# Kernel optimization log

Measured on AMD Instinct MI355X. Metric: run time of the kernel, lower is better.

Reference implementation:

```python
import jax, jax.numpy as jnp
import numpy as np

B, V, P, A, NF = 32, 2048, 64, 8, 128
F = P + A          # concat of transformed features and aggregator weights
DIN = P + 2 * A * F + A  # final cat: orig + expanded_collapsed + agg


def setup_inputs() -> dict:
    key = jax.random.key(0)
    ks = jax.random.split(key, 7)
    s = lambda fan: 1.0 / np.sqrt(fan)
    return {
        "vertices_in": jax.random.normal(ks[0], (B, V, P), dtype=jnp.float32),
        "W1": jax.random.normal(ks[1], (P, P), dtype=jnp.float32) * s(P),
        "b1": jax.random.normal(ks[2], (P,), dtype=jnp.float32) * s(P),
        "W2": jax.random.normal(ks[3], (P, A), dtype=jnp.float32) * s(P),
        "b2": jax.random.normal(ks[4], (A,), dtype=jnp.float32) * s(P),
        "Wout": jax.random.normal(ks[5], (DIN, NF), dtype=jnp.float32) * s(DIN),
        "bout": jax.random.normal(ks[6], (NF,), dtype=jnp.float32) * s(DIN),
    }


def reference(vertices_in, W1, b1, W2, b2, Wout, bout):
    # vertices_in: [B,V,P]
    vi = vertices_in @ W1 + b1                              # [B,V,P]
    agg = jnp.exp(-jnp.abs(vertices_in @ W2 + b2))          # [B,V,A] gauss_of_lin
    feats = jnp.concatenate([vi, agg], axis=-1)             # [B,V,F]
    # edge weights e[b,a,v] = agg[b,v,a]; broadcast multiply then max/mean over V
    prod = jnp.transpose(agg, (0, 2, 1))[:, :, :, None] * feats[:, None, :, :]  # [B,A,V,F]
    mx = jnp.max(prod, axis=2)                              # [B,A,F]
    mn = jnp.mean(prod, axis=2)                             # [B,A,F]
    collapsed = jnp.concatenate([mx, mn], axis=-1)          # [B,A,2F]
    # expand back to vertices: e[b,v,a] * collapsed[b,a,g]
    expanded = agg[:, :, :, None] * collapsed[:, None, :, :]  # [B,V,A,2F]
    expanded = expanded.reshape(B, V, A * 2 * F)
    x = jnp.concatenate([vertices_in, expanded, agg], axis=-1)  # [B,V,DIN]
    return jnp.tanh(x @ Wout + bout)                        # [B,V,NF]
```

## Files before the change

kernel.cpp:

```cpp
#include <hip/hip_runtime.h>
#include <math.h>

#define BB 32
#define VV 2048
#define PP 64
#define AA 8
#define NFF 128
#define FF 72
#define TWOF 144

__global__ __launch_bounds__(256) void k1_feats(
        const float* __restrict__ x,
        const float* __restrict__ W1, const float* __restrict__ b1,
        const float* __restrict__ W2, const float* __restrict__ b2,
        float* __restrict__ featsT, float* __restrict__ agg) {
    const int b    = blockIdx.y;
    const int t    = threadIdx.x;
    const int w    = __builtin_amdgcn_readfirstlane(t >> 6);
    const int lane = t & 63;
    const int v    = blockIdx.x * 64 + lane;

    float xs[64];
    const float4* xp = reinterpret_cast<const float4*>(x + ((size_t)b * VV + v) * PP);
    #pragma unroll
    for (int i = 0; i < 16; ++i) {
        float4 t4 = xp[i];
        xs[4 * i + 0] = t4.x; xs[4 * i + 1] = t4.y; xs[4 * i + 2] = t4.z; xs[4 * i + 3] = t4.w;
    }

    #pragma unroll 1
    for (int k = 0; k < 5; ++k) {
        const int c = w + 4 * k;
        if (c >= 18) break;
        const int f0 = 4 * c;
        float4 acc;
        if (c < 16) {
            acc = make_float4(b1[f0 + 0], b1[f0 + 1], b1[f0 + 2], b1[f0 + 3]);
            #pragma unroll
            for (int p = 0; p < 64; ++p) {
                const float4 wt = *reinterpret_cast<const float4*>(&W1[p * 64 + f0]);
                const float xv = xs[p];
                acc.x += xv * wt.x; acc.y += xv * wt.y; acc.z += xv * wt.z; acc.w += xv * wt.w;
            }
        } else {
            const int a0 = f0 - 64;
            acc = make_float4(b2[a0 + 0], b2[a0 + 1], b2[a0 + 2], b2[a0 + 3]);
            #pragma unroll
            for (int p = 0; p < 64; ++p) {
                const float4 wt = *reinterpret_cast<const float4*>(&W2[p * 8 + a0]);
                const float xv = xs[p];
                acc.x += xv * wt.x; acc.y += xv * wt.y; acc.z += xv * wt.z; acc.w += xv * wt.w;
            }
            acc.x = __expf(-fabsf(acc.x));
            acc.y = __expf(-fabsf(acc.y));
            acc.z = __expf(-fabsf(acc.z));
            acc.w = __expf(-fabsf(acc.w));
            float4* ap = reinterpret_cast<float4*>(agg + ((size_t)b * VV + v) * AA);
            ap[c - 16] = acc;
        }
        float* fr = featsT + ((size_t)b * FF + f0) * VV + v;
        fr[0 * VV] = acc.x; fr[1 * VV] = acc.y; fr[2 * VV] = acc.z; fr[3 * VV] = acc.w;
    }
}

__global__ __launch_bounds__(256) void k2_reduce(
        const float* __restrict__ featsT, const float* __restrict__ agg,
        float* __restrict__ collapsed) {
    const int fg = blockIdx.x;
    const int b  = blockIdx.y;
    const int f0 = fg * 4;
    const int t  = threadIdx.x;
    const int wave = t >> 6, lane = t & 63;

    __shared__ float redm[4][32];
    __shared__ float reds[4][32];

    float pmax[4][8], psum[4][8];
    #pragma unroll
    for (int j = 0; j < 4; ++j)
        #pragma unroll
        for (int a = 0; a < 8; ++a) { pmax[j][a] = -INFINITY; psum[j][a] = 0.0f; }

    for (int i = 0; i < 8; ++i) {
        const int v = i * 256 + t;
        const float4* ep = reinterpret_cast<const float4*>(agg + ((size_t)b * VV + v) * AA);
        const float4 e0 = ep[0], e1 = ep[1];
        float e[8];
        e[0] = e0.x; e[1] = e0.y; e[2] = e0.z; e[3] = e0.w;
        e[4] = e1.x; e[5] = e1.y; e[6] = e1.z; e[7] = e1.w;
        #pragma unroll
        for (int j = 0; j < 4; ++j) {
            const float fv = featsT[((size_t)b * FF + f0 + j) * VV + v];
            #pragma unroll
            for (int a = 0; a < 8; ++a) {
                const float pr = e[a] * fv;
                pmax[j][a] = fmaxf(pmax[j][a], pr);
                psum[j][a] += pr;
            }
        }
    }

    #pragma unroll
    for (int j = 0; j < 4; ++j) {
        #pragma unroll
        for (int a = 0; a < 8; ++a) {
            float m = pmax[j][a];
            float s = psum[j][a];
            #pragma unroll
            for (int d = 1; d < 64; d <<= 1) {
                m = fmaxf(m, __shfl_xor(m, d));
                s += __shfl_xor(s, d);
            }
            if (lane == 0) { redm[wave][j * 8 + a] = m; reds[wave][j * 8 + a] = s; }
        }
    }
    __syncthreads();

    if (t < 32) {
        const int j = t >> 3, a = t & 7;
        float m = redm[0][t], s = reds[0][t];
        #pragma unroll
        for (int w = 1; w < 4; ++w) { m = fmaxf(m, redm[w][t]); s += reds[w][t]; }
        float* cr = collapsed + ((size_t)b * AA + a) * TWOF;
        cr[f0 + j]      = m;
        cr[FF + f0 + j] = s * (1.0f / (float)VV);
    }
}

__global__ __launch_bounds__(256) void k2b_mprime(
        const float* __restrict__ collapsed, const float* __restrict__ Wout,
        float* __restrict__ Mp) {
    const int a = blockIdx.x, b = blockIdx.y;
    const int t = threadIdx.x;
    const int nf = t & 127, gh = t >> 7;
    __shared__ float part[2][128];

    const float* col  = collapsed + ((size_t)b * AA + a) * TWOF;
    const float* Wexp = Wout + (size_t)(64 + a * TWOF) * NFF;

    float acc = 0.0f;
    const int g0 = gh * 72;
    #pragma unroll 8
    for (int g = g0; g < g0 + 72; ++g)
        acc += col[g] * Wexp[(size_t)g * NFF + nf];
    part[gh][nf] = acc;
    __syncthreads();

    if (t < 128) {
        float r = part[0][t] + part[1][t] + Wout[(size_t)(1216 + a) * NFF + t];
        Mp[((size_t)b * AA + a) * NFF + t] = r;
    }
}

__device__ __forceinline__ float fast_tanh(float z) {
    const float e = __expf(2.0f * z);
    return 1.0f - 2.0f / (e + 1.0f);
}

__global__ __launch_bounds__(256) void k3_out(
        const float* __restrict__ x, const float* __restrict__ agg,
        const float* __restrict__ Mp, const float* __restrict__ Wout,
        const float* __restrict__ bout, float* __restrict__ out) {
    const int b    = blockIdx.y;
    const int t    = threadIdx.x;
    const int q    = __builtin_amdgcn_readfirstlane(t >> 6);
    const int lane = t & 63;
    const int v    = blockIdx.x * 64 + lane;
    const int n0   = q * 32;

    float xs[64];
    const float4* xp = reinterpret_cast<const float4*>(x + ((size_t)b * VV + v) * PP);
    #pragma unroll
    for (int i = 0; i < 16; ++i) {
        float4 t4 = xp[i];
        xs[4 * i + 0] = t4.x; xs[4 * i + 1] = t4.y; xs[4 * i + 2] = t4.z; xs[4 * i + 3] = t4.w;
    }
    float e[8];
    const float4* ep = reinterpret_cast<const float4*>(agg + ((size_t)b * VV + v) * AA);
    {
        const float4 e0 = ep[0], e1 = ep[1];
        e[0] = e0.x; e[1] = e0.y; e[2] = e0.z; e[3] = e0.w;
        e[4] = e1.x; e[5] = e1.y; e[6] = e1.z; e[7] = e1.w;
    }

    const float* Wq  = Wout + n0;
    const float* Mpq = Mp + (size_t)b * AA * NFF + n0;
    const float* bq  = bout + n0;
    float* op = out + ((size_t)b * VV + v) * NFF + n0;

    #pragma unroll 1
    for (int cc = 0; cc < 8; ++cc) {
        float4 acc = make_float4(bq[4 * cc + 0], bq[4 * cc + 1],
                                 bq[4 * cc + 2], bq[4 * cc + 3]);
        #pragma unroll
        for (int p = 0; p < 64; ++p) {
            const float4 wt = *reinterpret_cast<const float4*>(&Wq[(size_t)p * NFF + 4 * cc]);
            const float xv = xs[p];
            acc.x += xv * wt.x; acc.y += xv * wt.y; acc.z += xv * wt.z; acc.w += xv * wt.w;
        }
        #pragma unroll
        for (int a = 0; a < 8; ++a) {
            const float4 wt = *reinterpret_cast<const float4*>(&Mpq[(size_t)a * NFF + 4 * cc]);
            const float ea = e[a];
            acc.x += ea * wt.x; acc.y += ea * wt.y; acc.z += ea * wt.z; acc.w += ea * wt.w;
        }
        acc.x = fast_tanh(acc.x); acc.y = fast_tanh(acc.y);
        acc.z = fast_tanh(acc.z); acc.w = fast_tanh(acc.w);
        *reinterpret_cast<float4*>(&op[4 * cc]) = acc;
    }
}

extern "C" void kernel_launch(void* const* d_in, const int* in_sizes, int n_in,
                              void* d_out, int out_size, void* d_ws, size_t ws_size,
                              hipStream_t stream) {
    const float* x    = (const float*)d_in[0];
    const float* W1   = (const float*)d_in[1];
    const float* b1   = (const float*)d_in[2];
    const float* W2   = (const float*)d_in[3];
    const float* b2   = (const float*)d_in[4];
    const float* Wout = (const float*)d_in[5];
    const float* bout = (const float*)d_in[6];
    float* out = (float*)d_out;

    float* ws     = (float*)d_ws;
    float* featsT = ws;
    float* agg    = featsT + (size_t)BB * FF * VV;
    float* coll   = agg + (size_t)BB * VV * AA;
    float* Mp     = coll + (size_t)BB * AA * TWOF;

    k1_feats<<<dim3(32, 32), dim3(256), 0, stream>>>(x, W1, b1, W2, b2, featsT, agg);
    k2_reduce<<<dim3(18, 32), dim3(256), 0, stream>>>(featsT, agg, coll);
    k2b_mprime<<<dim3(8, 32), dim3(256), 0, stream>>>(coll, Wout, Mp);
    k3_out<<<dim3(32, 32), dim3(256), 0, stream>>>(x, agg, Mp, Wout, bout, out);
}
```

Before: 169.9 us.

## Split V-reduction across two blocks and restructure output GEMM loop order

```diff
diff --git a/kernel.cpp b/kernel.cpp
--- a/kernel.cpp
+++ b/kernel.cpp
@@ -65,8 +65,10 @@
 
 __global__ __launch_bounds__(256) void k2_reduce(
         const float* __restrict__ featsT, const float* __restrict__ agg,
-        float* __restrict__ collapsed) {
-    const int fg = blockIdx.x;
+        float* __restrict__ part) {
+    const int bx = blockIdx.x;
+    const int fg = bx >> 1;
+    const int vh = bx & 1;
     const int b  = blockIdx.y;
     const int f0 = fg * 4;
     const int t  = threadIdx.x;
@@ -81,8 +83,8 @@
         #pragma unroll
         for (int a = 0; a < 8; ++a) { pmax[j][a] = -INFINITY; psum[j][a] = 0.0f; }
 
-    for (int i = 0; i < 8; ++i) {
-        const int v = i * 256 + t;
+    for (int i = 0; i < 4; ++i) {
+        const int v = vh * 1024 + i * 256 + t;
         const float4* ep = reinterpret_cast<const float4*>(agg + ((size_t)b * VV + v) * AA);
         const float4 e0 = ep[0], e1 = ep[1];
         float e[8];
@@ -121,33 +123,45 @@
         float m = redm[0][t], s = reds[0][t];
         #pragma unroll
         for (int w = 1; w < 4; ++w) { m = fmaxf(m, redm[w][t]); s += reds[w][t]; }
-        float* cr = collapsed + ((size_t)b * AA + a) * TWOF;
-        cr[f0 + j]      = m;
-        cr[FF + f0 + j] = s * (1.0f / (float)VV);
+        float* pr = part + (((size_t)vh * BB + b) * AA + a) * TWOF;
+        pr[f0 + j]      = m;
+        pr[FF + f0 + j] = s;
     }
 }
 
 __global__ __launch_bounds__(256) void k2b_mprime(
-        const float* __restrict__ collapsed, const float* __restrict__ Wout,
+        const float* __restrict__ part, const float* __restrict__ Wout,
         float* __restrict__ Mp) {
     const int a = blockIdx.x, b = blockIdx.y;
     const int t = threadIdx.x;
     const int nf = t & 127, gh = t >> 7;
-    __shared__ float part[2][128];
-
-    const float* col  = collapsed + ((size_t)b * AA + a) * TWOF;
+    __shared__ float red[2][128];
+
+    const float* p0 = part + (((size_t)0 * BB + b) * AA + a) * TWOF;
+    const float* p1 = part + (((size_t)1 * BB + b) * AA + a) * TWOF;
     const float* Wexp = Wout + (size_t)(64 + a * TWOF) * NFF;
 
     float acc = 0.0f;
     const int g0 = gh * 72;
-    #pragma unroll 8
-    for (int g = g0; g < g0 + 72; ++g)
-        acc += col[g] * Wexp[(size_t)g * NFF + nf];
-    part[gh][nf] = acc;
+    if (gh == 0) {
+        #pragma unroll 8
+        for (int g = 0; g < 72; ++g) {
+            const float cg = fmaxf(p0[g], p1[g]);
+            acc += cg * Wexp[(size_t)g * NFF + nf];
+        }
+    } else {
+        #pragma unroll 8
+        for (int g = 72; g < 144; ++g) {
+            const float cg = (p0[g] + p1[g]) * (1.0f / (float)VV);
+            acc += cg * Wexp[(size_t)g * NFF + nf];
+        }
+    }
+    (void)g0;
+    red[gh][nf] = acc;
     __syncthreads();
 
     if (t < 128) {
-        float r = part[0][t] + part[1][t] + Wout[(size_t)(1216 + a) * NFF + t];
+        float r = red[0][t] + red[1][t] + Wout[(size_t)(1216 + a) * NFF + t];
         Mp[((size_t)b * AA + a) * NFF + t] = r;
     }
 }
@@ -168,13 +182,32 @@
     const int v    = blockIdx.x * 64 + lane;
     const int n0   = q * 32;
 
-    float xs[64];
+    const float* Wq  = Wout + n0;
+    const float* Mpq = Mp + (size_t)b * AA * NFF + n0;
+    const float* bq  = bout + n0;
+
+    float4 acc[8];
+    #pragma unroll
+    for (int cc = 0; cc < 8; ++cc)
+        acc[cc] = *reinterpret_cast<const float4*>(&bq[4 * cc]);
+
     const float4* xp = reinterpret_cast<const float4*>(x + ((size_t)b * VV + v) * PP);
-    #pragma unroll
+    #pragma unroll 4
     for (int i = 0; i < 16; ++i) {
-        float4 t4 = xp[i];
-        xs[4 * i + 0] = t4.x; xs[4 * i + 1] = t4.y; xs[4 * i + 2] = t4.z; xs[4 * i + 3] = t4.w;
-    }
+        const float4 xq = xp[i];
+        #pragma unroll
+        for (int pp = 0; pp < 4; ++pp) {
+            const float xv = (pp == 0) ? xq.x : (pp == 1) ? xq.y : (pp == 2) ? xq.z : xq.w;
+            const float* wrow = &Wq[(size_t)(4 * i + pp) * NFF];
+            #pragma unroll
+            for (int cc = 0; cc < 8; ++cc) {
+                const float4 wt = *reinterpret_cast<const float4*>(&wrow[4 * cc]);
+                acc[cc].x += xv * wt.x; acc[cc].y += xv * wt.y;
+                acc[cc].z += xv * wt.z; acc[cc].w += xv * wt.w;
+            }
+        }
+    }
+
     float e[8];
     const float4* ep = reinterpret_cast<const float4*>(agg + ((size_t)b * VV + v) * AA);
     {
@@ -182,32 +215,29 @@
         e[0] = e0.x; e[1] = e0.y; e[2] = e0.z; e[3] = e0.w;
         e[4] = e1.x; e[5] = e1.y; e[6] = e1.z; e[7] = e1.w;
     }
-
-    const float* Wq  = Wout + n0;
-    const float* Mpq = Mp + (size_t)b * AA * NFF + n0;
-    const float* bq  = bout + n0;
+    #pragma unroll
+    for (int a = 0; a < 8; ++a) {
+        const float ea = e[a];
+        const float* mrow = &Mpq[(size_t)a * NFF];
+        #pragma unroll
+        for (int cc = 0; cc < 8; ++cc) {
+            const float4 wt = *reinterpret_cast<const float4*>(&mrow[4 * cc]);
+            acc[cc].x += ea * wt.x; acc[cc].y += ea * wt.y;
+            acc[cc].z += ea * wt.z; acc[cc].w += ea * wt.w;
+        }
+    }
+
     float* op = out + ((size_t)b * VV + v) * NFF + n0;
-
-    #pragma unroll 1
+    #pragma unroll
     for (int cc = 0; cc < 8; ++cc) {
-        float4 acc = make_float4(bq[4 * cc + 0], bq[4 * cc + 1],
-                                 bq[4 * cc + 2], bq[4 * cc + 3]);
-        #pragma unroll
-        for (int p = 0; p < 64; ++p) {
-            const float4 wt = *reinterpret_cast<const float4*>(&Wq[(size_t)p * NFF + 4 * cc]);
-            const float xv = xs[p];
-            acc.x += xv * wt.x; acc.y += xv * wt.y; acc.z += xv * wt.z; acc.w += xv * wt.w;
-        }
-        #pragma unroll
-        for (int a = 0; a < 8; ++a) {
-            const float4 wt = *reinterpret_cast<const float4*>(&Mpq[(size_t)a * NFF + 4 * cc]);
-            const float ea = e[a];
-            acc.x += ea * wt.x; acc.y += ea * wt.y; acc.z += ea * wt.z; acc.w += ea * wt.w;
-        }
-        acc.x = fast_tanh(acc.x); acc.y = fast_tanh(acc.y);
-        acc.z = fast_tanh(acc.z); acc.w = fast_tanh(acc.w);
-        *reinterpret_cast<float4*>(&op[4 * cc]) = acc;
-    }
+        float4 r = acc[cc];
+        r.x = fast_tanh(r.x); r.y = fast_tanh(r.y);
+        r.z = fast_tanh(r.z); r.w = fast_tanh(r.w);
+        acc[cc] = r;
+    }
+    #pragma unroll
+    for (int cc = 0; cc < 8; ++cc)
+        *reinterpret_cast<float4*>(&op[4 * cc]) = acc[cc];
 }
 
 extern "C" void kernel_launch(void* const* d_in, const int* in_sizes, int n_in,
@@ -225,11 +255,11 @@
     float* ws     = (float*)d_ws;
     float* featsT = ws;
     float* agg    = featsT + (size_t)BB * FF * VV;
-    float* coll   = agg + (size_t)BB * VV * AA;
-    float* Mp     = coll + (size_t)BB * AA * TWOF;
+    float* part   = agg + (size_t)BB * VV * AA;
+    float* Mp     = part + (size_t)2 * BB * AA * TWOF;
 
     k1_feats<<<dim3(32, 32), dim3(256), 0, stream>>>(x, W1, b1, W2, b2, featsT, agg);
-    k2_reduce<<<dim3(18, 32), dim3(256), 0, stream>>>(featsT, agg, coll);
-    k2b_mprime<<<dim3(8, 32), dim3(256), 0, stream>>>(coll, Wout, Mp);
+    k2_reduce<<<dim3(36, 32), dim3(256), 0, stream>>>(featsT, agg, part);
+    k2b_mprime<<<dim3(8, 32), dim3(256), 0, stream>>>(part, Wout, Mp);
     k3_out<<<dim3(32, 32), dim3(256), 0, stream>>>(x, agg, Mp, Wout, bout, out);
 }
```

New measurement: 174.3 us. +2.6%, slower.
